# Kernel tuning notes

Hardware: AMD Instinct MI355X
Metric: run time of the kernel (lower is better)

## Reference

```python
import jax, jax.numpy as jnp
import numpy as np

B, T, O, D, H = 8, 256, 16, 512, 8
HD = D // H
EPS = 1e-5


def setup_inputs() -> dict:
    key = jax.random.key(0)
    ks = jax.random.split(key, 12)
    s = 1.0 / np.sqrt(D)
    inp = {
        "organ_states": jax.random.normal(ks[0], (B, T, O, D), dtype=jnp.float32),
        "organ_mask": jax.random.randint(ks[1], (B, T, O), 0, 2) > 0,
        "Wq": jax.random.uniform(ks[2], (D, D), jnp.float32, -s, s),
        "bq": jnp.zeros((D,), jnp.float32),
        "Wk": jax.random.uniform(ks[3], (D, D), jnp.float32, -s, s),
        "bk": jnp.zeros((D,), jnp.float32),
        "Wv": jax.random.uniform(ks[4], (D, D), jnp.float32, -s, s),
        "bv": jnp.zeros((D,), jnp.float32),
        "Wo": jax.random.uniform(ks[5], (D, D), jnp.float32, -s, s),
        "bo": jnp.zeros((D,), jnp.float32),
        "gamma": jnp.ones((D,), jnp.float32),
        "beta": jnp.zeros((D,), jnp.float32),
    }
    return inp


def reference(organ_states, organ_mask, Wq, bq, Wk, bk, Wv, bv, Wo, bo, gamma, beta):
    x = organ_states  # (B, T, O, D)
    b, t, o, d = x.shape

    def heads(y):  # (B,T,O,D) -> (B,O,H,T,HD)
        return y.reshape(b, t, o, H, HD).transpose(0, 2, 3, 1, 4)

    q = heads(jnp.einsum('btod,de->btoe', x, Wq) + bq)
    k = heads(jnp.einsum('btod,de->btoe', x, Wk) + bk)
    v = heads(jnp.einsum('btod,de->btoe', x, Wv) + bv)

    scores = jnp.einsum('bohqd,bohkd->bohqk', q, k) / np.sqrt(HD).astype(np.float32)
    # key mask: (B,T,O) -> (B,O,1,1,T)
    mk = organ_mask.transpose(0, 2, 1)[:, :, None, None, :]
    scores = jnp.where(mk, scores, -jnp.inf)
    attn = jax.nn.softmax(scores, axis=-1)
    attn = jnp.where(mk, attn, 0.0)

    att = jnp.einsum('bohqk,bohkd->bohqd', attn, v)  # (B,O,H,T,HD)
    att = att.transpose(0, 3, 1, 2, 4).reshape(b, t, o, d)  # (B,T,O,D)

    out = jnp.einsum('btod,de->btoe', att, Wo) + bo
    res = out + x
    mu = jnp.mean(res, axis=-1, keepdims=True)
    var = jnp.mean(jnp.square(res - mu), axis=-1, keepdims=True)
    y = (res - mu) / jnp.sqrt(var + EPS) * gamma + beta
    y = y * organ_mask[..., None].astype(y.dtype)
    return y
```

## Files before the change

kernel.cpp:

```cpp
#include <hip/hip_runtime.h>


typedef __attribute__((ext_vector_type(8))) short bf16x8;
typedef __attribute__((ext_vector_type(4))) float f32x4;

#define MFMA16(a, b, c) __builtin_amdgcn_mfma_f32_16x16x32_bf16((a), (b), (c), 0, 0, 0)

__device__ __forceinline__ unsigned short f2bf(float f) {
  unsigned int u = __builtin_bit_cast(unsigned int, f);
  u += 0x7fffu + ((u >> 16) & 1u);
  return (unsigned short)(u >> 16);
}

__device__ __forceinline__ void gload_lds16(const void* g, void* lds) {
  __builtin_amdgcn_global_load_lds((__attribute__((address_space(1))) void*)g,
                                   (__attribute__((address_space(3))) void*)lds,
                                   16, 0, 0);
}

#define WS_XB   0ull
#define WS_WT   33554432ull
#define WS_Q    35651584ull
#define WS_K    69206016ull
#define WS_V    102760448ull
#define WS_MASK 136314880ull

__global__ void k_cvt_x(const float* __restrict__ x, unsigned short* __restrict__ xb) {
  int i = blockIdx.x * 256 + threadIdx.x;
  float4 v = ((const float4*)x)[i];
  ushort4 o;
  o.x = f2bf(v.x); o.y = f2bf(v.y); o.z = f2bf(v.z); o.w = f2bf(v.w);
  ((ushort4*)xb)[i] = o;
}

__global__ void k_prep_w(const float* __restrict__ Wq, const float* __restrict__ Wk,
                         const float* __restrict__ Wv, const float* __restrict__ Wo,
                         unsigned short* __restrict__ Wt) {
  int ep = blockIdx.x;
  const float* src; int e;
  if (ep < 512)       { src = Wq; e = ep; }
  else if (ep < 1024) { src = Wk; e = ep - 512; }
  else if (ep < 1536) { src = Wv; e = ep - 1024; }
  else                { src = Wo; e = ep - 1536; }
  for (int d = threadIdx.x; d < 512; d += 256)
    Wt[(size_t)ep * 512 + d] = f2bf(src[(size_t)d * 512 + e]);
}

__global__ void k_prep_mask(const void* __restrict__ mraw, unsigned char* __restrict__ mout) {
  const unsigned int* u = (const unsigned int*)mraw;
  int lane = threadIdx.x & 63;
  int packed = __any(u[lane] > 1u);
  int idx = blockIdx.x * 256 + threadIdx.x;
  unsigned char m;
  if (packed) m = ((const unsigned char*)mraw)[idx] ? 1 : 0;
  else        m = u[idx] ? 1 : 0;
  mout[idx] = m;
}

__global__ __launch_bounds__(512) void k_qkv(
    const unsigned short* __restrict__ Xb, const unsigned short* __restrict__ Wt,
    const float* __restrict__ bq, const float* __restrict__ bk, const float* __restrict__ bv,
    unsigned short* __restrict__ Qb, unsigned short* __restrict__ Kb, unsigned short* __restrict__ Vb) {
  __shared__ char sm[73728];
  const int tid = threadIdx.x, l = tid & 63, w = tid >> 6;
  const int lane15 = l & 15, quad = l >> 4;
  const int rbase = blockIdx.x * 64, which = blockIdx.y;
  const char* xg = (const char*)Xb;
  const char* wgp = (const char*)(Wt + (size_t)which * 512 * 512);
  const int srow = tid >> 3;
  const int c16 = (tid & 7) * 16;
  const int swz_a = c16 ^ ((srow & 7) << 4);
  char* adst = sm + w * 1024;
  f32x4 acc[4][4] = {};
  for (int ks = 0; ks < 8; ++ks) {
    __syncthreads();
    gload_lds16(xg + (size_t)(rbase + srow) * 1024 + ks * 128 + swz_a, adst);
#pragma unroll
    for (int p = 0; p < 8; ++p) {
      int er = p * 64 + srow;
      gload_lds16(wgp + (size_t)er * 1024 + ks * 128 + (c16 ^ ((er & 7) << 4)),
                  sm + 8192 + p * 8192 + w * 1024);
    }
    __syncthreads();
#pragma unroll
    for (int kc = 0; kc < 2; ++kc) {
      bf16x8 af[4], bfr[4];
#pragma unroll
      for (int mt = 0; mt < 4; ++mt) {
        int row = mt * 16 + lane15;
        int byt = (row * 128 + kc * 64 + quad * 16) ^ ((row & 7) << 4);
        af[mt] = *(const bf16x8*)(sm + byt);
      }
#pragma unroll
      for (int nt = 0; nt < 4; ++nt) {
        int col = w * 64 + nt * 16 + lane15;
        int byt = (col * 128 + kc * 64 + quad * 16) ^ ((col & 7) << 4);
        bfr[nt] = *(const bf16x8*)(sm + 8192 + byt);
      }
#pragma unroll
      for (int mt = 0; mt < 4; ++mt)
#pragma unroll
        for (int nt = 0; nt < 4; ++nt)
          acc[mt][nt] = MFMA16(af[mt], bfr[nt], acc[mt][nt]);
    }
  }
  const float* bias = (which == 0) ? bq : (which == 1) ? bk : bv;
  unsigned short* dst = (which == 0) ? Qb : (which == 1) ? Kb : Vb;
#pragma unroll
  for (int mt = 0; mt < 4; ++mt) {
#pragma unroll
    for (int reg = 0; reg < 4; ++reg) {
      int r = rbase + mt * 16 + quad * 4 + reg;
      int b = r >> 12, t = (r >> 4) & 255, o = r & 15;
      size_t base_bt = (size_t)((b * 16 + o) * 8 + w) * 16384 + (size_t)t * 64;
#pragma unroll
      for (int nt = 0; nt < 4; ++nt) {
        int e = w * 64 + nt * 16 + lane15;
        float v = acc[mt][nt][reg] + bias[e];
        dst[base_bt + nt * 16 + lane15] = f2bf(v);
      }
    }
  }
}

__global__ __launch_bounds__(512, 2) void k_attn(
    const unsigned short* __restrict__ Qb, const unsigned short* __restrict__ Kb,
    const unsigned short* __restrict__ Vb, const unsigned char* __restrict__ Mc,
    unsigned short* __restrict__ att) {
  __shared__ char sm[99328];
  const int tid = threadIdx.x, l = tid & 63, w = tid >> 6;
  const int lane15 = l & 15, quad = l >> 4;
  const int bid = blockIdx.x;
  const int h = bid & 7, o = (bid >> 3) & 15, b = bid >> 7;
  const size_t head = (size_t)((b * 16 + o) * 8 + h) * 16384;
  const unsigned short* qh = Qb + head;
  const char* kg = (const char*)(Kb + head);
  const unsigned short* vh = Vb + head;

  {
    const int srow = tid >> 3;
    const int c16 = (tid & 7) * 16;
    char* kdst = sm + w * 1024;
#pragma unroll
    for (int i = 0; i < 4; ++i) {
      int t = i * 64 + srow;
      gload_lds16(kg + (size_t)t * 128 + (c16 ^ ((t & 7) << 4)), kdst + i * 8192);
    }
  }
  const int q0 = w * 32;
  bf16x8 qf[2][2];
#pragma unroll
  for (int mt = 0; mt < 2; ++mt)
#pragma unroll
    for (int kc = 0; kc < 2; ++kc)
      qf[mt][kc] = *(const bf16x8*)(qh + (size_t)(q0 + mt * 16 + lane15) * 64 + kc * 32 + quad * 8);
  unsigned short vreg[32];
  {
    const int hd = tid & 63, tq = tid >> 6;
#pragma unroll
    for (int i = 0; i < 4; ++i)
#pragma unroll
      for (int j = 0; j < 8; ++j)
        vreg[i * 8 + j] = vh[(size_t)(tq * 32 + i * 8 + j) * 64 + hd];
  }
  float* maskb = (float*)(sm + 98304);
  if (tid < 256)
    maskb[tid] = Mc[(size_t)(b * 256 + tid) * 16 + o] ? 0.0f : -43280.0f;
  {
    const int hd = tid & 63, tq = tid >> 6;
    const int rowb = 32768 + hd * 512;
    const int swz = (hd & 7) << 4;
#pragma unroll
    for (int i = 0; i < 4; ++i) {
      bf16x8 pk;
#pragma unroll
      for (int j = 0; j < 8; ++j) pk[j] = (short)vreg[i * 8 + j];
      int t0 = tq * 32 + i * 8;
      *(bf16x8*)(sm + rowb + ((t0 * 2) ^ swz)) = pk;
    }
  }
  __syncthreads();

  f32x4 sacc[2][16] = {};
#pragma unroll
  for (int c = 0; c < 4; ++c) {
#pragma unroll
    for (int kc = 0; kc < 2; ++kc) {
      bf16x8 kf[4];
#pragma unroll
      for (int nt = 0; nt < 4; ++nt) {
        int t = c * 64 + nt * 16 + lane15;
        int byt = t * 128 + ((kc * 64 + quad * 16) ^ ((t & 7) << 4));
        kf[nt] = *(const bf16x8*)(sm + byt);
      }
#pragma unroll
      for (int mt = 0; mt < 2; ++mt)
#pragma unroll
        for (int nt = 0; nt < 4; ++nt)
          sacc[mt][c * 4 + nt] = MFMA16(qf[mt][kc], kf[nt], sacc[mt][c * 4 + nt]);
    }
  }

  float biasv[16];
#pragma unroll
  for (int g = 0; g < 16; ++g) biasv[g] = maskb[g * 16 + lane15];
  float inv[2][4];
#pragma unroll
  for (int mt = 0; mt < 2; ++mt) {
#pragma unroll
    for (int reg = 0; reg < 4; ++reg) {
      float v[16];
#pragma unroll
      for (int g = 0; g < 16; ++g)
        v[g] = sacc[mt][g][reg] * 0.18033688f + biasv[g];
      float m = v[0];
#pragma unroll
      for (int g = 1; g < 16; ++g) m = fmaxf(m, v[g]);
#pragma unroll
      for (int d = 1; d < 16; d <<= 1) m = fmaxf(m, __shfl_xor(m, d));
      float rs = 0.f;
#pragma unroll
      for (int g = 0; g < 16; ++g) {
        float p = __builtin_amdgcn_exp2f(v[g] - m);
        sacc[mt][g][reg] = p;
        rs += p;
      }
#pragma unroll
      for (int d = 1; d < 16; d <<= 1) rs += __shfl_xor(rs, d);
      inv[mt][reg] = 1.0f / rs;
    }
  }

  char* pb = sm + 65536 + w * 4096;
  f32x4 pv[2][4] = {};
#pragma unroll
  for (int c = 0; c < 4; ++c) {
#pragma unroll
    for (int mt = 0; mt < 2; ++mt)
#pragma unroll
      for (int nt = 0; nt < 4; ++nt)
#pragma unroll
        for (int reg = 0; reg < 4; ++reg) {
          int qrow = mt * 16 + quad * 4 + reg;
          int byt = (qrow * 128 + (nt * 16 + lane15) * 2) ^ ((qrow & 7) << 4);
          *(unsigned short*)(pb + byt) = f2bf(sacc[mt][c * 4 + nt][reg]);
        }
#pragma unroll
    for (int kc = 0; kc < 2; ++kc) {
      bf16x8 pa[2], vbr[4];
#pragma unroll
      for (int mt = 0; mt < 2; ++mt) {
        int qrow = mt * 16 + lane15;
        int byt = (qrow * 128 + kc * 64 + quad * 16) ^ ((qrow & 7) << 4);
        pa[mt] = *(const bf16x8*)(pb + byt);
      }
#pragma unroll
      for (int nh = 0; nh < 4; ++nh) {
        int hd = nh * 16 + lane15;
        int byt = hd * 512 + ((c * 128 + kc * 64 + quad * 16) ^ ((hd & 7) << 4));
        vbr[nh] = *(const bf16x8*)(sm + 32768 + byt);
      }
#pragma unroll
      for (int mt = 0; mt < 2; ++mt)
#pragma unroll
        for (int nh = 0; nh < 4; ++nh)
          pv[mt][nh] = MFMA16(pa[mt], vbr[nh], pv[mt][nh]);
    }
  }

#pragma unroll
  for (int mt = 0; mt < 2; ++mt) {
#pragma unroll
    for (int reg = 0; reg < 4; ++reg) {
      int q = q0 + mt * 16 + quad * 4 + reg;
      size_t r = (size_t)(b * 256 + q) * 16 + o;
      float iv = inv[mt][reg];
#pragma unroll
      for (int nh = 0; nh < 4; ++nh)
        att[r * 512 + h * 64 + nh * 16 + lane15] = f2bf(pv[mt][nh][reg] * iv);
    }
  }
}

__global__ __launch_bounds__(512) void k_oproj(
    const unsigned short* __restrict__ A, const unsigned short* __restrict__ Wt,
    const float* __restrict__ bo, const float* __restrict__ X,
    const unsigned char* __restrict__ Mc, const float* __restrict__ gamma,
    const float* __restrict__ beta, float* __restrict__ out) {
  __shared__ char sm[73728];
  __shared__ float psum[64][8];
  __shared__ float psumsq[64][8];
  __shared__ float smean[64];
  __shared__ float srstd[64];
  const int tid = threadIdx.x, l = tid & 63, w = tid >> 6;
  const int lane15 = l & 15, quad = l >> 4;
  const int rbase = blockIdx.x * 64;
  const char* ag = (const char*)A;
  const char* wgp = (const char*)(Wt + (size_t)1536 * 512);
  const int srow = tid >> 3;
  const int c16 = (tid & 7) * 16;
  const int swz_a = c16 ^ ((srow & 7) << 4);
  char* adst = sm + w * 1024;
  f32x4 acc[4][4] = {};
  for (int ks = 0; ks < 8; ++ks) {
    __syncthreads();
    gload_lds16(ag + (size_t)(rbase + srow) * 1024 + ks * 128 + swz_a, adst);
#pragma unroll
    for (int p = 0; p < 8; ++p) {
      int er = p * 64 + srow;
      gload_lds16(wgp + (size_t)er * 1024 + ks * 128 + (c16 ^ ((er & 7) << 4)),
                  sm + 8192 + p * 8192 + w * 1024);
    }
    __syncthreads();
#pragma unroll
    for (int kc = 0; kc < 2; ++kc) {
      bf16x8 af[4], bfr[4];
#pragma unroll
      for (int mt = 0; mt < 4; ++mt) {
        int row = mt * 16 + lane15;
        int byt = (row * 128 + kc * 64 + quad * 16) ^ ((row & 7) << 4);
        af[mt] = *(const bf16x8*)(sm + byt);
      }
#pragma unroll
      for (int nt = 0; nt < 4; ++nt) {
        int col = w * 64 + nt * 16 + lane15;
        int byt = (col * 128 + kc * 64 + quad * 16) ^ ((col & 7) << 4);
        bfr[nt] = *(const bf16x8*)(sm + 8192 + byt);
      }
#pragma unroll
      for (int mt = 0; mt < 4; ++mt)
#pragma unroll
        for (int nt = 0; nt < 4; ++nt)
          acc[mt][nt] = MFMA16(af[mt], bfr[nt], acc[mt][nt]);
    }
  }
#pragma unroll
  for (int mt = 0; mt < 4; ++mt) {
#pragma unroll
    for (int reg = 0; reg < 4; ++reg) {
      int rl = mt * 16 + quad * 4 + reg;
      int r = rbase + rl;
      float s1 = 0.f, s2 = 0.f;
#pragma unroll
      for (int nt = 0; nt < 4; ++nt) {
        int col = w * 64 + nt * 16 + lane15;
        float v = acc[mt][nt][reg] + bo[col] + X[(size_t)r * 512 + col];
        acc[mt][nt][reg] = v;
        s1 += v; s2 += v * v;
      }
#pragma unroll
      for (int d = 1; d < 16; d <<= 1) { s1 += __shfl_xor(s1, d); s2 += __shfl_xor(s2, d); }
      if (lane15 == 0) { psum[rl][w] = s1; psumsq[rl][w] = s2; }
    }
  }
  __syncthreads();
  if (tid < 64) {
    float a = 0.f, q = 0.f;
#pragma unroll
    for (int j = 0; j < 8; ++j) { a += psum[tid][j]; q += psumsq[tid][j]; }
    float mu = a * (1.f / 512.f);
    float var = q * (1.f / 512.f) - mu * mu;
    smean[tid] = mu;
    srstd[tid] = rsqrtf(fmaxf(var, 0.f) + 1e-5f);
  }
  __syncthreads();
#pragma unroll
  for (int mt = 0; mt < 4; ++mt) {
#pragma unroll
    for (int reg = 0; reg < 4; ++reg) {
      int rl = mt * 16 + quad * 4 + reg;
      int r = rbase + rl;
      float mu = smean[rl], rs = srstd[rl];
      float mkf = Mc[r] ? 1.f : 0.f;
#pragma unroll
      for (int nt = 0; nt < 4; ++nt) {
        int col = w * 64 + nt * 16 + lane15;
        float y = (acc[mt][nt][reg] - mu) * rs * gamma[col] + beta[col];
        out[(size_t)r * 512 + col] = y * mkf;
      }
    }
  }
}

extern "C" void kernel_launch(void* const* d_in, const int* in_sizes, int n_in,
                              void* d_out, int out_size, void* d_ws, size_t ws_size,
                              hipStream_t stream) {
  const float* X     = (const float*)d_in[0];
  const void*  Mraw  = d_in[1];
  const float* Wq    = (const float*)d_in[2];
  const float* bq    = (const float*)d_in[3];
  const float* Wk    = (const float*)d_in[4];
  const float* bk    = (const float*)d_in[5];
  const float* Wv    = (const float*)d_in[6];
  const float* bv    = (const float*)d_in[7];
  const float* Wo    = (const float*)d_in[8];
  const float* bo    = (const float*)d_in[9];
  const float* gamma = (const float*)d_in[10];
  const float* beta  = (const float*)d_in[11];

  char* ws = (char*)d_ws;
  unsigned short* Xb  = (unsigned short*)(ws + WS_XB);
  unsigned short* Wt  = (unsigned short*)(ws + WS_WT);
  unsigned short* Qb  = (unsigned short*)(ws + WS_Q);
  unsigned short* Kb  = (unsigned short*)(ws + WS_K);
  unsigned short* Vb  = (unsigned short*)(ws + WS_V);
  unsigned char*  Mc  = (unsigned char*)(ws + WS_MASK);
  unsigned short* att = Xb;

  hipLaunchKernelGGL(k_cvt_x,    dim3(16384),   dim3(256), 0, stream, X, Xb);
  hipLaunchKernelGGL(k_prep_w,   dim3(2048),    dim3(256), 0, stream, Wq, Wk, Wv, Wo, Wt);
  hipLaunchKernelGGL(k_prep_mask,dim3(128),     dim3(256), 0, stream, Mraw, Mc);
  hipLaunchKernelGGL(k_qkv,      dim3(512, 3),  dim3(512), 0, stream, Xb, Wt, bq, bk, bv, Qb, Kb, Vb);
  hipLaunchKernelGGL(k_attn,     dim3(1024),    dim3(512), 0, stream, Qb, Kb, Vb, Mc, att);
  hipLaunchKernelGGL(k_oproj,    dim3(512),     dim3(512), 0, stream, att, Wt, bo, X, Mc, gamma, beta,
                     (float*)d_out);
}
```

Before: 295.1 us.

## Fuse X bf16 conversion into QKV GEMM, retile GEMM, and tile weight transpose

Removes the standalone X fp32-to-bf16 conversion kernel; the QKV GEMM now reads fp32 X directly and converts it with packed bf16 conversion while staging into LDS. The QKV GEMM is retiled to 128x128 output tiles with 256 threads and a swizzled block order, so each block covers a 128-row slice of one Q/K/V matrix instead of full 512-wide N. The weight transpose kernel now uses an LDS 64x64 tile for coalesced reads and writes. The trade-off is that X is re-read in fp32 once per N tile (12 times), which costs more global traffic than reading bf16 three times.

```diff
diff --git a/kernel.cpp b/kernel.cpp
--- a/kernel.cpp
+++ b/kernel.cpp
@@ -12,38 +12,54 @@
   return (unsigned short)(u >> 16);
 }
 
+__device__ __forceinline__ unsigned int cvt_pk_bf16(float lo, float hi) {
+  unsigned int r;
+  asm("v_cvt_pk_bf16_f32 %0, %1, %2" : "=v"(r) : "v"(lo), "v"(hi));
+  return r;
+}
+
 __device__ __forceinline__ void gload_lds16(const void* g, void* lds) {
   __builtin_amdgcn_global_load_lds((__attribute__((address_space(1))) void*)g,
                                    (__attribute__((address_space(3))) void*)lds,
                                    16, 0, 0);
 }
 
-#define WS_XB   0ull
+#define WS_ATT  0ull
 #define WS_WT   33554432ull
 #define WS_Q    35651584ull
 #define WS_K    69206016ull
 #define WS_V    102760448ull
 #define WS_MASK 136314880ull
 
-__global__ void k_cvt_x(const float* __restrict__ x, unsigned short* __restrict__ xb) {
-  int i = blockIdx.x * 256 + threadIdx.x;
-  float4 v = ((const float4*)x)[i];
-  ushort4 o;
-  o.x = f2bf(v.x); o.y = f2bf(v.y); o.z = f2bf(v.z); o.w = f2bf(v.w);
-  ((ushort4*)xb)[i] = o;
-}
-
 __global__ void k_prep_w(const float* __restrict__ Wq, const float* __restrict__ Wk,
                          const float* __restrict__ Wv, const float* __restrict__ Wo,
                          unsigned short* __restrict__ Wt) {
-  int ep = blockIdx.x;
-  const float* src; int e;
-  if (ep < 512)       { src = Wq; e = ep; }
-  else if (ep < 1024) { src = Wk; e = ep - 512; }
-  else if (ep < 1536) { src = Wv; e = ep - 1024; }
-  else                { src = Wo; e = ep - 1536; }
-  for (int d = threadIdx.x; d < 512; d += 256)
-    Wt[(size_t)ep * 512 + d] = f2bf(src[(size_t)d * 512 + e]);
+  __shared__ float tl[64][65];
+  const float* src = blockIdx.z == 0 ? Wq : blockIdx.z == 1 ? Wk : blockIdx.z == 2 ? Wv : Wo;
+  const int d0 = blockIdx.x * 64, e0 = blockIdx.y * 64;
+  const int tid = threadIdx.x;
+  {
+    const int dr = tid >> 2, ec = (tid & 3) * 16;
+    const float4* srow = (const float4*)(src + (size_t)(d0 + dr) * 512 + e0 + ec);
+#pragma unroll
+    for (int j = 0; j < 4; ++j) {
+      float4 v = srow[j];
+      tl[dr][ec + j * 4 + 0] = v.x;
+      tl[dr][ec + j * 4 + 1] = v.y;
+      tl[dr][ec + j * 4 + 2] = v.z;
+      tl[dr][ec + j * 4 + 3] = v.w;
+    }
+  }
+  __syncthreads();
+  const int dd0 = (tid & 7) * 8;
+#pragma unroll
+  for (int i = 0; i < 2; ++i) {
+    int e = i * 32 + (tid >> 3);
+    bf16x8 ob;
+#pragma unroll
+    for (int j = 0; j < 8; ++j) ob[j] = (short)f2bf(tl[dd0 + j][e]);
+    *(bf16x8*)(Wt + ((size_t)blockIdx.z * 512 + e0 + e) * 512 + d0 + dd0) = ob;
+  }
 }
 
 __global__ void k_prep_mask(const void* __restrict__ mraw, unsigned char* __restrict__ mout) {
@@ -57,29 +73,44 @@
   mout[idx] = m;
 }
 
-__global__ __launch_bounds__(512) void k_qkv(
-    const unsigned short* __restrict__ Xb, const unsigned short* __restrict__ Wt,
+__global__ __launch_bounds__(256) void k_qkv(
+    const float* __restrict__ X, const unsigned short* __restrict__ Wt,
     const float* __restrict__ bq, const float* __restrict__ bk, const float* __restrict__ bv,
     unsigned short* __restrict__ Qb, unsigned short* __restrict__ Kb, unsigned short* __restrict__ Vb) {
-  __shared__ char sm[73728];
+  __shared__ char sm[32768];
   const int tid = threadIdx.x, l = tid & 63, w = tid >> 6;
   const int lane15 = l & 15, quad = l >> 4;
-  const int rbase = blockIdx.x * 64, which = blockIdx.y;
-  const char* xg = (const char*)Xb;
-  const char* wgp = (const char*)(Wt + (size_t)which * 512 * 512);
+  const int flat = blockIdx.x;
+  const int swz = (flat & 7) * 384 + (flat >> 3);
+  const int mtile = swz & 255, yb = swz >> 8;
+  const int which = yb >> 2, ntile = yb & 3;
+  const int rbase = mtile * 128;
+  const unsigned short* wgp = Wt + ((size_t)which * 512 + ntile * 128) * 512;
+  const int wr = w >> 1, wc = w & 1;
   const int srow = tid >> 3;
   const int c16 = (tid & 7) * 16;
-  const int swz_a = c16 ^ ((srow & 7) << 4);
-  char* adst = sm + w * 1024;
+  char* const abase = sm;
+  char* const bbase = sm + 16384;
   f32x4 acc[4][4] = {};
   for (int ks = 0; ks < 8; ++ks) {
     __syncthreads();
-    gload_lds16(xg + (size_t)(rbase + srow) * 1024 + ks * 128 + swz_a, adst);
-#pragma unroll
-    for (int p = 0; p < 8; ++p) {
-      int er = p * 64 + srow;
-      gload_lds16(wgp + (size_t)er * 1024 + ks * 128 + (c16 ^ ((er & 7) << 4)),
-                  sm + 8192 + p * 8192 + w * 1024);
+#pragma unroll
+    for (int i = 0; i < 4; ++i) {
+      int row = i * 32 + srow;
+      gload_lds16((const char*)wgp + (size_t)row * 1024 + ks * 128 + (c16 ^ ((row & 7) << 4)),
+                  bbase + i * 4096 + w * 1024);
+    }
+#pragma unroll
+    for (int i = 0; i < 4; ++i) {
+      int row = i * 32 + srow;
+      const float4* xs = (const float4*)(X + (size_t)(rbase + row) * 512 + ks * 64 + (tid & 7) * 8);
+      float4 v0 = xs[0], v1 = xs[1];
+      uint4 pk;
+      pk.x = cvt_pk_bf16(v0.x, v0.y);
+      pk.y = cvt_pk_bf16(v0.z, v0.w);
+      pk.z = cvt_pk_bf16(v1.x, v1.y);
+      pk.w = cvt_pk_bf16(v1.z, v1.w);
+      *(uint4*)(abase + row * 128 + (c16 ^ ((row & 7) << 4))) = pk;
     }
     __syncthreads();
 #pragma unroll
@@ -87,15 +118,13 @@
       bf16x8 af[4], bfr[4];
 #pragma unroll
       for (int mt = 0; mt < 4; ++mt) {
-        int row = mt * 16 + lane15;
-        int byt = (row * 128 + kc * 64 + quad * 16) ^ ((row & 7) << 4);
-        af[mt] = *(const bf16x8*)(sm + byt);
-      }
-#pragma unroll
-      for (int nt = 0; nt < 4; ++nt) {
-        int col = w * 64 + nt * 16 + lane15;
-        int byt = (col * 128 + kc * 64 + quad * 16) ^ ((col & 7) << 4);
-        bfr[nt] = *(const bf16x8*)(sm + 8192 + byt);
+        int row = wr * 64 + mt * 16 + lane15;
+        af[mt] = *(const bf16x8*)(abase + row * 128 + ((kc * 64 + quad * 16) ^ ((row & 7) << 4)));
+      }
+#pragma unroll
+      for (int nt = 0; nt < 4; ++nt) {
+        int col = wc * 64 + nt * 16 + lane15;
+        bfr[nt] = *(const bf16x8*)(bbase + col * 128 + ((kc * 64 + quad * 16) ^ ((col & 7) << 4)));
       }
 #pragma unroll
       for (int mt = 0; mt < 4; ++mt)
@@ -106,18 +135,18 @@
   }
   const float* bias = (which == 0) ? bq : (which == 1) ? bk : bv;
   unsigned short* dst = (which == 0) ? Qb : (which == 1) ? Kb : Vb;
+  const int h = ntile * 2 + wc;
 #pragma unroll
   for (int mt = 0; mt < 4; ++mt) {
 #pragma unroll
     for (int reg = 0; reg < 4; ++reg) {
-      int r = rbase + mt * 16 + quad * 4 + reg;
+      int r = rbase + wr * 64 + mt * 16 + quad * 4 + reg;
       int b = r >> 12, t = (r >> 4) & 255, o = r & 15;
-      size_t base_bt = (size_t)((b * 16 + o) * 8 + w) * 16384 + (size_t)t * 64;
-#pragma unroll
-      for (int nt = 0; nt < 4; ++nt) {
-        int e = w * 64 + nt * 16 + lane15;
-        float v = acc[mt][nt][reg] + bias[e];
-        dst[base_bt + nt * 16 + lane15] = f2bf(v);
+      size_t base_bt = (size_t)((b * 16 + o) * 8 + h) * 16384 + (size_t)t * 64;
+#pragma unroll
+      for (int nt = 0; nt < 4; ++nt) {
+        int hd = nt * 16 + lane15;
+        dst[base_bt + hd] = f2bf(acc[mt][nt][reg] + bias[h * 64 + hd]);
       }
     }
   }
@@ -399,18 +428,16 @@
   const float* beta  = (const float*)d_in[11];
 
   char* ws = (char*)d_ws;
-  unsigned short* Xb  = (unsigned short*)(ws + WS_XB);
+  unsigned short* att = (unsigned short*)(ws + WS_ATT);
   unsigned short* Wt  = (unsigned short*)(ws + WS_WT);
   unsigned short* Qb  = (unsigned short*)(ws + WS_Q);
   unsigned short* Kb  = (unsigned short*)(ws + WS_K);
   unsigned short* Vb  = (unsigned short*)(ws + WS_V);
   unsigned char*  Mc  = (unsigned char*)(ws + WS_MASK);
-  unsigned short* att = Xb;
-
-  hipLaunchKernelGGL(k_cvt_x,    dim3(16384),   dim3(256), 0, stream, X, Xb);
-  hipLaunchKernelGGL(k_prep_w,   dim3(2048),    dim3(256), 0, stream, Wq, Wk, Wv, Wo, Wt);
+
+  hipLaunchKernelGGL(k_prep_w,   dim3(8, 8, 4), dim3(256), 0, stream, Wq, Wk, Wv, Wo, Wt);
   hipLaunchKernelGGL(k_prep_mask,dim3(128),     dim3(256), 0, stream, Mraw, Mc);
-  hipLaunchKernelGGL(k_qkv,      dim3(512, 3),  dim3(512), 0, stream, Xb, Wt, bq, bk, bv, Qb, Kb, Vb);
+  hipLaunchKernelGGL(k_qkv,      dim3(3072),    dim3(256), 0, stream, X, Wt, bq, bk, bv, Qb, Kb, Vb);
   hipLaunchKernelGGL(k_attn,     dim3(1024),    dim3(512), 0, stream, Qb, Kb, Vb, Mc, att);
   hipLaunchKernelGGL(k_oproj,    dim3(512),     dim3(512), 0, stream, att, Wt, bo, X, Mc, gamma, beta,
                      (float*)d_out);
```

Measured after the change: 328.7 us. 11.4% more time.
